# Performance work log

Measured on AMD Instinct MI355X. Metric: run time of the kernel, lower is better.

The kernel has to match this reference:

```python
import jax, jax.numpy as jnp
import numpy as np

N, E, K = 20000, 320000, 4
IN, HID, OUT, HD = 512, 256, 128, 256


def setup_inputs() -> dict:
    key = jax.random.key(0)
    ks = jax.random.split(key, 12)
    def lin(k, fi, fo):
        return jax.random.normal(k, (fi, fo), jnp.float32) / np.sqrt(fi)
    return {
        "x": jax.random.normal(ks[0], (N, IN), jnp.float32),
        "edge_index": jax.random.randint(ks[1], (K, 2, E), 0, N),
        "value": jax.random.normal(ks[2], (K, 3), jnp.float32),
        "index": jax.random.randint(ks[3], (K, 2), 0, N),
        "W1": lin(ks[4], IN, HID),  "b1": jnp.zeros((HID,), jnp.float32),
        "W2": lin(ks[5], HID, OUT), "b2": jnp.zeros((OUT,), jnp.float32),
        "Wd": lin(ks[6], 2 * OUT + 3, HD), "bd": jnp.zeros((HD,), jnp.float32),
        "Wp": lin(ks[7], HD, 1),    "bp": jnp.zeros((1,), jnp.float32),
    }


def reference(x, edge_index, value, index, W1, b1, W2, b2, Wd, bd, Wp, bp):
    n = x.shape[0]
    loops = jnp.arange(n)

    def gcn(h, src, dst, W, b):
        # GCNConv: symmetric normalization with self-loops already in src/dst
        deg = jnp.zeros((n,), h.dtype).at[dst].add(1.0)
        dinv = jnp.where(deg > 0, deg ** -0.5, 0.0)
        norm = dinv[src] * dinv[dst]                      # [E+N]
        msg = (h @ W)[src] * norm[:, None]                # [E+N, F_out]
        return jnp.zeros((n, W.shape[1]), h.dtype).at[dst].add(msg) + b

    def encode(ei):
        src = jnp.concatenate([ei[0], loops])             # add self-loops
        dst = jnp.concatenate([ei[1], loops])
        h = jax.nn.relu(gcn(x, src, dst, W1, b1))
        return gcn(h, src, dst, W2, b2)                   # [N, OUT]

    def step(carry, inp):
        ei, val, idx = inp
        mu = encode(ei)
        h = jnp.concatenate([mu[idx[0]], mu[idx[1]], val])  # [2*OUT+3]
        o = jax.nn.relu(h @ Wd + bd)
        p = jax.nn.sigmoid(o @ Wp + bp)
        return carry, p[0]

    _, preds = jax.lax.scan(step, None, (edge_index, value, index))
    return preds  # [K]
```

## Files before the change

### kernel.cpp

```cpp
#include <hip/hip_runtime.h>
#include <hip/hip_bf16.h>


#define NN 20000
#define EE 320000
#define E4 (EE/4)
#define KK 4
#define FIN 512
#define FHID 256
#define FOUT 128
#define FHD 256
#define NH (2*FOUT+3)
#define CAP1 1024
#define MS2 128
#define BCAP 256
#define BMW 640

__device__ __forceinline__ float dinvf(int indeg) {
  return rsqrtf((float)(indeg + 1));
}

__global__ __launch_bounds__(256) void kz_zero(int4* __restrict__ p, int n4) {
  int i = blockIdx.x * 256 + threadIdx.x;
  if (i < n4) p[i] = make_int4(0, 0, 0, 0);
}

__global__ __launch_bounds__(256) void k12_scan_claim(const int* __restrict__ ei,
                                                      const int* __restrict__ idx,
                                                      int* __restrict__ cnt1,
                                                      int* __restrict__ L1src,
                                                      int* __restrict__ L1sel,
                                                      int* __restrict__ reg,
                                                      int* __restrict__ slotNode,
                                                      int* __restrict__ mslots,
                                                      unsigned* __restrict__ bA) {
  int k = blockIdx.y;
  int* rk = reg + (size_t)k * NN;
  unsigned* bAk = bA + k * BMW;
  int t0 = idx[2 * k], t1 = idx[2 * k + 1];
  if (blockIdx.x == 0 && threadIdx.x < 2) {
    int node = (threadIdx.x == 0) ? t0 : t1;
    if (atomicCAS(&rk[node], 0, -2) == 0) {
      int s = atomicAdd(&mslots[k], 1);
      if (s < MS2) {
        slotNode[k * MS2 + s] = node; rk[node] = s + 1;
        atomicOr(&bAk[node >> 5], 1u << (node & 31));
      }
    }
  }
  int e4 = blockIdx.x * blockDim.x + threadIdx.x;
  if (e4 >= E4) return;
  const int* srcp = ei + (size_t)k * 2 * EE;
  int4 d4 = ((const int4*)(srcp + EE))[e4];
  int ds[4] = {d4.x, d4.y, d4.z, d4.w};
  #pragma unroll
  for (int c = 0; c < 4; c++) {
    bool h0 = (ds[c] == t0), h1 = (ds[c] == t1);
    if (h0 || h1) {
      int u = srcp[e4 * 4 + c];
      if (h0) {
        int p = atomicAdd(&cnt1[k], 1);
        if (p < CAP1) { L1src[k * CAP1 + p] = u; L1sel[k * CAP1 + p] = 0; }
      }
      if (h1) {
        int p = atomicAdd(&cnt1[k], 1);
        if (p < CAP1) { L1src[k * CAP1 + p] = u; L1sel[k * CAP1 + p] = 1; }
      }
      if (atomicCAS(&rk[u], 0, -2) == 0) {
        int s = atomicAdd(&mslots[k], 1);
        if (s < MS2) {
          slotNode[k * MS2 + s] = u; rk[u] = s + 1;
          atomicOr(&bAk[u >> 5], 1u << (u & 31));
        }
      }
    }
  }
}

__global__ __launch_bounds__(256) void k3_scanL2(const int* __restrict__ ei,
                                                 const int* __restrict__ reg,
                                                 const unsigned* __restrict__ bA,
                                                 unsigned* __restrict__ bB,
                                                 int* __restrict__ bcnt,
                                                 int* __restrict__ bucket) {
  __shared__ unsigned lbA[BMW];
  int k = blockIdx.y;
  const unsigned* bAk = bA + k * BMW;
  for (int i = threadIdx.x; i < BMW; i += 256) lbA[i] = bAk[i];
  __syncthreads();
  int e4 = blockIdx.x * blockDim.x + threadIdx.x;
  if (e4 >= E4) return;
  const int* srcp = ei + (size_t)k * 2 * EE;
  int4 d4 = ((const int4*)(srcp + EE))[e4];
  const int* rk = reg + (size_t)k * NN;
  unsigned* bBk = bB + k * BMW;
  int ds[4] = {d4.x, d4.y, d4.z, d4.w};
  #pragma unroll
  for (int c = 0; c < 4; c++) {
    int d = ds[c];
    if ((lbA[d >> 5] >> (d & 31)) & 1u) {
      int s = rk[d] - 1;
      int u = srcp[e4 * 4 + c];
      int p = atomicAdd(&bcnt[k * MS2 + s], 1);
      if (p < BCAP) bucket[((size_t)k * MS2 + s) * BCAP + p] = u;
      atomicOr(&bBk[u >> 5], 1u << (u & 31));
    }
  }
}

__global__ __launch_bounds__(256) void k4_deg(const int* __restrict__ ei,
                                              const unsigned* __restrict__ bB,
                                              int* __restrict__ deg) {
  __shared__ unsigned lbB[BMW];
  int k = blockIdx.y;
  const unsigned* bBk = bB + k * BMW;
  for (int i = threadIdx.x; i < BMW; i += 256) lbB[i] = bBk[i];
  __syncthreads();
  int e4 = blockIdx.x * blockDim.x + threadIdx.x;
  if (e4 >= E4) return;
  const int4* dst4 = (const int4*)(ei + (size_t)k * 2 * EE + EE);
  int4 d4 = dst4[e4];
  int ds[4] = {d4.x, d4.y, d4.z, d4.w};
  #pragma unroll
  for (int c = 0; c < 4; c++) {
    int d = ds[c];
    if ((lbB[d >> 5] >> (d & 31)) & 1u) atomicAdd(&deg[k * NN + d], 1);
  }
}

__global__ __launch_bounds__(256) void k5a_gemv1(const int* __restrict__ slotNode,
                                                 const int* __restrict__ mslots,
                                                 const int* __restrict__ bcnt,
                                                 const int* __restrict__ bucket,
                                                 const int* __restrict__ deg,
                                                 const float* __restrict__ x,
                                                 const float* __restrict__ W1,
                                                 float* __restrict__ partQ) {
  __shared__ int   uS[BCAP];
  __shared__ float duS[BCAP];
  __shared__ float aggq[128];
  __shared__ float gtmp[128];
  int k = blockIdx.y;
  int s = blockIdx.x >> 2, q = blockIdx.x & 3;
  if (s >= mslots[k]) return;
  int tid = threadIdx.x;
  int node = slotNode[k * MS2 + s];
  int rawbc = bcnt[k * MS2 + s];
  int nb = min(rawbc, BCAP);
  const int* bk = bucket + ((size_t)k * MS2 + s) * BCAP;
  if (tid < nb) {
    int u = bk[tid];
    uS[tid] = u;
    duS[tid] = dinvf(deg[k * NN + u]);
  }
  __syncthreads();
  float dn = dinvf(rawbc);
  int f = tid & 127, g = tid >> 7;
  const float* xq = x + q * 128 + f;
  float a = (g == 0) ? dn * xq[(size_t)node * FIN] : 0.f;
  for (int e = g; e < nb; e += 2) a += duS[e] * xq[(size_t)uS[e] * FIN];
  if (g == 1) gtmp[f] = a;
  __syncthreads();
  if (g == 0) aggq[f] = dn * (a + gtmp[f]);
  __syncthreads();
  float acc = 0.f;
  const float* w1p = W1 + (size_t)(q * 128) * FHID + tid;
  #pragma unroll 8
  for (int kk = 0; kk < 128; kk++) acc += aggq[kk] * w1p[(size_t)kk * FHID];
  partQ[(((size_t)k * MS2 + s) * 4 + q) * FHID + tid] = acc;
}

__global__ __launch_bounds__(256) void k5b_gemv2(const int* __restrict__ mslots,
                                                 const float* __restrict__ partQ,
                                                 const float* __restrict__ b1,
                                                 const float* __restrict__ W2,
                                                 float* __restrict__ HW2) {
  __shared__ float hrow[FHID];
  __shared__ float pr[FHID];
  int k = blockIdx.y, s = blockIdx.x;
  if (s >= mslots[k]) return;
  int tid = threadIdx.x;
  const float* pq = partQ + (((size_t)k * MS2 + s) * 4) * FHID;
  {
    float v = pq[tid] + pq[FHID + tid] + pq[2 * FHID + tid] + pq[3 * FHID + tid] + b1[tid];
    hrow[tid] = v > 0.f ? v : 0.f;
  }
  __syncthreads();
  int half = tid >> 7, j = tid & 127;
  float a = 0.f;
  const float* w2p = W2 + (size_t)(half * 128) * FOUT + j;
  #pragma unroll 8
  for (int kk = 0; kk < 128; kk++) a += hrow[half * 128 + kk] * w2p[(size_t)kk * FOUT];
  pr[tid] = a;
  __syncthreads();
  if (half == 0) HW2[((size_t)k * MS2 + s) * FOUT + j] = pr[j] + pr[128 + j];
}

__global__ __launch_bounds__(1024) void k6_decode(const float* __restrict__ HW2,
                                                  const float* __restrict__ b2,
                                                  const int* __restrict__ cnt1,
                                                  const int* __restrict__ L1src,
                                                  const int* __restrict__ L1sel,
                                                  const int* __restrict__ idx,
                                                  const int* __restrict__ reg,
                                                  const int* __restrict__ bcnt,
                                                  const float* __restrict__ value,
                                                  const float* __restrict__ Wd,
                                                  const float* __restrict__ bd,
                                                  const float* __restrict__ Wp,
                                                  const float* __restrict__ bp,
                                                  float* __restrict__ out) {
  __shared__ float hD[NH + 1];
  __shared__ float oD[FHD];
  __shared__ float pd[4][FHD];
  __shared__ float red[4];
  int k = blockIdx.x;
  int tid = threadIdx.x;
  const int* rk = reg + (size_t)k * NN;
  int n1 = min(cnt1[k], CAP1);
  if (tid < 256) {
    int tsel = tid >> 7, j = tid & 127;
    int t = idx[2 * k + tsel];
    int tslot = rk[t] - 1;
    float dit = dinvf(bcnt[k * MS2 + tslot]);
    float acc = b2[j] + dit * dit * HW2[((size_t)k * MS2 + tslot) * FOUT + j];
    for (int i = 0; i < n1; i++) {
      if (L1sel[k * CAP1 + i] == tsel) {
        int sn = L1src[k * CAP1 + i];
        int ss = rk[sn] - 1;
        float dis = dinvf(bcnt[k * MS2 + ss]);
        acc += dis * dit * HW2[((size_t)k * MS2 + ss) * FOUT + j];
      }
    }
    hD[tsel * FOUT + j] = acc;
    if (tid < 3) hD[2 * FOUT + tid] = value[k * 3 + tid];
  }
  __syncthreads();
  {
    int jj = tid & 255, qd = tid >> 8;
    int i0 = qd * 65, i1 = min(NH, i0 + 65);
    float a2 = (qd == 0) ? bd[jj] : 0.f;
    for (int i = i0; i < i1; i++) a2 += hD[i] * Wd[(size_t)i * FHD + jj];
    pd[qd][jj] = a2;
  }
  __syncthreads();
  if (tid < FHD) {
    float v = pd[0][tid] + pd[1][tid] + pd[2][tid] + pd[3][tid];
    oD[tid] = v > 0.f ? v : 0.f;
  }
  __syncthreads();
  if (tid < FHD) {
    float r = oD[tid] * Wp[tid];
    for (int o2 = 32; o2 > 0; o2 >>= 1) r += __shfl_down(r, o2);
    if ((tid & 63) == 0) red[tid >> 6] = r;
  }
  __syncthreads();
  if (tid == 0) {
    float ssum = red[0] + red[1] + red[2] + red[3] + bp[0];
    out[k] = 1.f / (1.f + expf(-ssum));
  }
}

extern "C" void kernel_launch(void* const* d_in, const int* in_sizes, int n_in,
                              void* d_out, int out_size, void* d_ws, size_t ws_size,
                              hipStream_t stream) {
  const float* x     = (const float*)d_in[0];
  const int*   ei    = (const int*)d_in[1];
  const float* value = (const float*)d_in[2];
  const int*   idx   = (const int*)d_in[3];
  const float* W1    = (const float*)d_in[4];
  const float* b1    = (const float*)d_in[5];
  const float* W2    = (const float*)d_in[6];
  const float* b2    = (const float*)d_in[7];
  const float* Wd    = (const float*)d_in[8];
  const float* bd    = (const float*)d_in[9];
  const float* Wp    = (const float*)d_in[10];
  const float* bp    = (const float*)d_in[11];
  float* out = (float*)d_out;

  char* ws = (char*)d_ws;
  size_t off = 0;
  auto alloc = [&](size_t bytes) -> void* {
    void* p = ws + off;
    off = (off + bytes + 255) & ~(size_t)255;
    return p;
  };
  size_t zints = (size_t)(2 * KK * NN + 2 * KK * BMW + KK * MS2 + 2 * KK);
  int* reg   = (int*)alloc(zints * sizeof(int));
  int* deg   = reg + KK * NN;
  unsigned* bA = (unsigned*)(deg + KK * NN);
  unsigned* bB = bA + KK * BMW;
  int* bcnt  = (int*)(bB + KK * BMW);
  int* cnt1  = bcnt + KK * MS2;
  int* mslots = cnt1 + KK;
  size_t zbytes = zints * sizeof(int);
  int* L1src = (int*)alloc((size_t)KK * CAP1 * sizeof(int));
  int* L1sel = (int*)alloc((size_t)KK * CAP1 * sizeof(int));
  int* slotNode = (int*)alloc((size_t)KK * MS2 * sizeof(int));
  int* bucket = (int*)alloc((size_t)KK * MS2 * BCAP * sizeof(int));
  float* HW2 = (float*)alloc((size_t)KK * MS2 * FOUT * sizeof(float));
  float* partQ = (float*)alloc((size_t)KK * MS2 * 4 * FHID * sizeof(float));
  (void)ws_size; (void)in_sizes; (void)n_in; (void)out_size;

  int n4 = (int)((zbytes + 15) / 16);
  dim3 escan((E4 + 255) / 256, KK);

  kz_zero<<<(n4 + 255) / 256, 256, 0, stream>>>((int4*)reg, n4);
  k12_scan_claim<<<escan, 256, 0, stream>>>(ei, idx, cnt1, L1src, L1sel,
                                            reg, slotNode, mslots, bA);
  k3_scanL2<<<escan, 256, 0, stream>>>(ei, reg, bA, bB, bcnt, bucket);
  k4_deg<<<escan, 256, 0, stream>>>(ei, bB, deg);
  k5a_gemv1<<<dim3(MS2 * 4, KK), 256, 0, stream>>>(slotNode, mslots, bcnt, bucket,
                                                   deg, x, W1, partQ);
  k5b_gemv2<<<dim3(MS2, KK), 256, 0, stream>>>(mslots, partQ, b1, W2, HW2);
  k6_decode<<<dim3(KK), 1024, 0, stream>>>(HW2, b2, cnt1, L1src, L1sel, idx, reg,
                                           bcnt, value, Wd, bd, Wp, bp, out);
}
```

Measured before the change: 60.57 us.

## Fold decoder Wd projection into per-slot GEMV and precompute b2·Wd

Uses linearity to push the decoder's first linear layer (Wd) through the second GCN aggregation. Each slot's HW2 row is multiplied by both halves of Wd inside the parallel k5b kernel, and b2·Wd is precomputed in extra blocks of the zeroing kernel. The decode kernel then only does a weighted sum of precomputed 256-wide rows per neighbor. This removes the serial 259x256 GEMV done by a single 1024-thread block per k, at the cost of two more 128x256 GEMVs per slot and a larger intermediate buffer.

```diff
diff --git a/kernel.cpp b/kernel.cpp
--- a/kernel.cpp
+++ b/kernel.cpp
@@ -20,9 +20,24 @@
   return rsqrtf((float)(indeg + 1));
 }
 
-__global__ __launch_bounds__(256) void kz_zero(int4* __restrict__ p, int n4) {
-  int i = blockIdx.x * 256 + threadIdx.x;
-  if (i < n4) p[i] = make_int4(0, 0, 0, 0);
+__global__ __launch_bounds__(256) void kz_zero(int4* __restrict__ p, int n4,
+                                               const float* __restrict__ b2,
+                                               const float* __restrict__ Wd,
+                                               float* __restrict__ b2Wd) {
+  int nzb = (n4 + 255) >> 8;
+  int b = blockIdx.x;
+  if (b < nzb) {
+    int i = b * 256 + threadIdx.x;
+    if (i < n4) p[i] = make_int4(0, 0, 0, 0);
+    return;
+  }
+  int half = b - nzb;
+  int jj = threadIdx.x;
+  float acc = 0.f;
+  const float* wd = Wd + (size_t)(half * 128) * FHD + jj;
+  #pragma unroll 8
+  for (int kk = 0; kk < 128; kk++) acc += b2[kk] * wd[(size_t)kk * FHD];
+  b2Wd[half * FHD + jj] = acc;
 }
 
 __global__ __launch_bounds__(256) void k12_scan_claim(const int* __restrict__ ei,
@@ -174,9 +189,11 @@
                                                  const float* __restrict__ partQ,
                                                  const float* __restrict__ b1,
                                                  const float* __restrict__ W2,
-                                                 float* __restrict__ HW2) {
+                                                 const float* __restrict__ Wd,
+                                                 float* __restrict__ Yd) {
   __shared__ float hrow[FHID];
   __shared__ float pr[FHID];
+  __shared__ float hw2S[FOUT];
   int k = blockIdx.y, s = blockIdx.x;
   if (s >= mslots[k]) return;
   int tid = threadIdx.x;
@@ -193,67 +210,64 @@
   for (int kk = 0; kk < 128; kk++) a += hrow[half * 128 + kk] * w2p[(size_t)kk * FOUT];
   pr[tid] = a;
   __syncthreads();
-  if (half == 0) HW2[((size_t)k * MS2 + s) * FOUT + j] = pr[j] + pr[128 + j];
-}
-
-__global__ __launch_bounds__(1024) void k6_decode(const float* __restrict__ HW2,
-                                                  const float* __restrict__ b2,
-                                                  const int* __restrict__ cnt1,
-                                                  const int* __restrict__ L1src,
-                                                  const int* __restrict__ L1sel,
-                                                  const int* __restrict__ idx,
-                                                  const int* __restrict__ reg,
-                                                  const int* __restrict__ bcnt,
-                                                  const float* __restrict__ value,
-                                                  const float* __restrict__ Wd,
-                                                  const float* __restrict__ bd,
-                                                  const float* __restrict__ Wp,
-                                                  const float* __restrict__ bp,
-                                                  float* __restrict__ out) {
-  __shared__ float hD[NH + 1];
-  __shared__ float oD[FHD];
-  __shared__ float pd[4][FHD];
+  if (half == 0) hw2S[j] = pr[j] + pr[128 + j];
+  __syncthreads();
+  float y0 = 0.f, y1 = 0.f;
+  const float* wd0 = Wd + tid;
+  const float* wd1 = Wd + (size_t)128 * FHD + tid;
+  #pragma unroll 4
+  for (int kk = 0; kk < FOUT; kk++) {
+    float hv = hw2S[kk];
+    y0 += hv * wd0[(size_t)kk * FHD];
+    y1 += hv * wd1[(size_t)kk * FHD];
+  }
+  float* ydp = Yd + ((size_t)(k * MS2 + s) * 2) * FHD;
+  ydp[tid] = y0;
+  ydp[FHD + tid] = y1;
+}
+
+__global__ __launch_bounds__(256) void k6_decode(const float* __restrict__ Yd,
+                                                 const float* __restrict__ b2Wd,
+                                                 const int* __restrict__ cnt1,
+                                                 const int* __restrict__ L1src,
+                                                 const int* __restrict__ L1sel,
+                                                 const int* __restrict__ idx,
+                                                 const int* __restrict__ reg,
+                                                 const int* __restrict__ bcnt,
+                                                 const float* __restrict__ value,
+                                                 const float* __restrict__ Wd,
+                                                 const float* __restrict__ bd,
+                                                 const float* __restrict__ Wp,
+                                                 const float* __restrict__ bp,
+                                                 float* __restrict__ out) {
   __shared__ float red[4];
   int k = blockIdx.x;
   int tid = threadIdx.x;
   const int* rk = reg + (size_t)k * NN;
   int n1 = min(cnt1[k], CAP1);
-  if (tid < 256) {
-    int tsel = tid >> 7, j = tid & 127;
-    int t = idx[2 * k + tsel];
-    int tslot = rk[t] - 1;
-    float dit = dinvf(bcnt[k * MS2 + tslot]);
-    float acc = b2[j] + dit * dit * HW2[((size_t)k * MS2 + tslot) * FOUT + j];
-    for (int i = 0; i < n1; i++) {
-      if (L1sel[k * CAP1 + i] == tsel) {
-        int sn = L1src[k * CAP1 + i];
-        int ss = rk[sn] - 1;
-        float dis = dinvf(bcnt[k * MS2 + ss]);
-        acc += dis * dit * HW2[((size_t)k * MS2 + ss) * FOUT + j];
-      }
-    }
-    hD[tsel * FOUT + j] = acc;
-    if (tid < 3) hD[2 * FOUT + tid] = value[k * 3 + tid];
-  }
-  __syncthreads();
-  {
-    int jj = tid & 255, qd = tid >> 8;
-    int i0 = qd * 65, i1 = min(NH, i0 + 65);
-    float a2 = (qd == 0) ? bd[jj] : 0.f;
-    for (int i = i0; i < i1; i++) a2 += hD[i] * Wd[(size_t)i * FHD + jj];
-    pd[qd][jj] = a2;
-  }
-  __syncthreads();
-  if (tid < FHD) {
-    float v = pd[0][tid] + pd[1][tid] + pd[2][tid] + pd[3][tid];
-    oD[tid] = v > 0.f ? v : 0.f;
-  }
-  __syncthreads();
-  if (tid < FHD) {
-    float r = oD[tid] * Wp[tid];
-    for (int o2 = 32; o2 > 0; o2 >>= 1) r += __shfl_down(r, o2);
-    if ((tid & 63) == 0) red[tid >> 6] = r;
-  }
+  int t0 = idx[2 * k], t1 = idx[2 * k + 1];
+  int ts0 = rk[t0] - 1, ts1 = rk[t1] - 1;
+  float dit0 = dinvf(bcnt[k * MS2 + ts0]);
+  float dit1 = dinvf(bcnt[k * MS2 + ts1]);
+  float acc = bd[tid] + b2Wd[tid] + b2Wd[FHD + tid];
+  acc += value[3 * k + 0] * Wd[(size_t)256 * FHD + tid]
+       + value[3 * k + 1] * Wd[(size_t)257 * FHD + tid]
+       + value[3 * k + 2] * Wd[(size_t)258 * FHD + tid];
+  const float* ydb = Yd + (size_t)k * MS2 * 2 * FHD;
+  acc += dit0 * dit0 * ydb[(size_t)ts0 * 2 * FHD + tid];
+  acc += dit1 * dit1 * ydb[(size_t)ts1 * 2 * FHD + FHD + tid];
+  for (int i = 0; i < n1; i++) {
+    int sn = L1src[k * CAP1 + i];
+    int ts = L1sel[k * CAP1 + i];
+    int ss = rk[sn] - 1;
+    float dis = dinvf(bcnt[k * MS2 + ss]);
+    float dit = ts ? dit1 : dit0;
+    acc += dis * dit * ydb[((size_t)ss * 2 + ts) * FHD + tid];
+  }
+  float o = acc > 0.f ? acc : 0.f;
+  float r = o * Wp[tid];
+  for (int o2 = 32; o2 > 0; o2 >>= 1) r += __shfl_down(r, o2);
+  if ((tid & 63) == 0) red[tid >> 6] = r;
   __syncthreads();
   if (tid == 0) {
     float ssum = red[0] + red[1] + red[2] + red[3] + bp[0];
@@ -298,21 +312,23 @@
   int* L1sel = (int*)alloc((size_t)KK * CAP1 * sizeof(int));
   int* slotNode = (int*)alloc((size_t)KK * MS2 * sizeof(int));
   int* bucket = (int*)alloc((size_t)KK * MS2 * BCAP * sizeof(int));
-  float* HW2 = (float*)alloc((size_t)KK * MS2 * FOUT * sizeof(float));
   float* partQ = (float*)alloc((size_t)KK * MS2 * 4 * FHID * sizeof(float));
+  float* Yd = (float*)alloc((size_t)KK * MS2 * 2 * FHD * sizeof(float));
+  float* b2Wd = (float*)alloc((size_t)2 * FHD * sizeof(float));
   (void)ws_size; (void)in_sizes; (void)n_in; (void)out_size;
 
   int n4 = (int)((zbytes + 15) / 16);
+  int nzb = (n4 + 255) / 256;
   dim3 escan((E4 + 255) / 256, KK);
 
-  kz_zero<<<(n4 + 255) / 256, 256, 0, stream>>>((int4*)reg, n4);
+  kz_zero<<<nzb + 2, 256, 0, stream>>>((int4*)reg, n4, b2, Wd, b2Wd);
   k12_scan_claim<<<escan, 256, 0, stream>>>(ei, idx, cnt1, L1src, L1sel,
                                             reg, slotNode, mslots, bA);
   k3_scanL2<<<escan, 256, 0, stream>>>(ei, reg, bA, bB, bcnt, bucket);
   k4_deg<<<escan, 256, 0, stream>>>(ei, bB, deg);
   k5a_gemv1<<<dim3(MS2 * 4, KK), 256, 0, stream>>>(slotNode, mslots, bcnt, bucket,
                                                    deg, x, W1, partQ);
-  k5b_gemv2<<<dim3(MS2, KK), 256, 0, stream>>>(mslots, partQ, b1, W2, HW2);
-  k6_decode<<<dim3(KK), 1024, 0, stream>>>(HW2, b2, cnt1, L1src, L1sel, idx, reg,
-                                           bcnt, value, Wd, bd, Wp, bp, out);
-}
+  k5b_gemv2<<<dim3(MS2, KK), 256, 0, stream>>>(mslots, partQ, b1, W2, Wd, Yd);
+  k6_decode<<<dim3(KK), 256, 0, stream>>>(Yd, b2Wd, cnt1, L1src, L1sel, idx, reg,
+                                          bcnt, value, Wd, bd, Wp, bp, out);
+}
```

Result: slower. 62.64 us (+3.4%).
